# Performance work log

Measured on AMD Instinct MI355X. Metric: run time of the kernel, lower is better.

Reference implementation:

```python
import jax, jax.numpy as jnp
import numpy as np

NPOINT = 1024
RADIUS = 0.2
NSAMPLE = 64
BN_EPS = 1e-5


def setup_inputs() -> dict:
    key = jax.random.key(0)
    ks = jax.random.split(key, 16)
    B, N = 8, 8192
    inp = {
        "xyz": jax.random.normal(ks[0], (B, 3, N), jnp.float32),
        "points": jax.random.normal(ks[1], (B, 3, N), jnp.float32),
        "seed_inds": jax.random.randint(ks[2], (B, N), 0, N),
    }
    chans = [6, 64, 64, 128]
    for i in range(3):
        cin, cout = chans[i], chans[i + 1]
        kk = jax.random.split(ks[3 + i], 3)
        inp[f"w{i}"] = jax.random.normal(kk[0], (cout, cin), jnp.float32) / np.sqrt(cin)
        inp[f"b{i}"] = jnp.zeros((cout,), jnp.float32)
        inp[f"g{i}"] = jnp.ones((cout,), jnp.float32)
        inp[f"be{i}"] = jnp.zeros((cout,), jnp.float32)
        inp[f"m{i}"] = jax.random.normal(kk[1], (cout,), jnp.float32) * 0.1
        inp[f"v{i}"] = jax.random.uniform(kk[2], (cout,), jnp.float32, 0.5, 1.5)
    return inp


def _fps(xyz, npoint):
    # xyz: [B, N, 3]. Deterministic start at index 0 (torch uses a random start).
    B, N, _ = xyz.shape

    def step(carry, _):
        dist, far = carry
        cent = jnp.take_along_axis(xyz, far[:, None, None], axis=1)  # [B,1,3]
        d = jnp.sum((xyz - cent) ** 2, -1)                           # [B,N]
        dist = jnp.minimum(dist, d)
        nxt = jnp.argmax(dist, -1)
        return (dist, nxt), far

    init = (jnp.full((B, N), 1e10, xyz.dtype), jnp.zeros((B,), jnp.int32))
    _, idxs = jax.lax.scan(step, init, None, length=npoint)
    return idxs.T  # [B, npoint]


def _sqdist(src, dst):
    # src [B,S,3], dst [B,N,3] -> [B,S,N]
    d = -2.0 * jnp.einsum("bsc,bnc->bsn", src, dst)
    d += jnp.sum(src ** 2, -1)[:, :, None]
    d += jnp.sum(dst ** 2, -1)[:, None, :]
    return d


def _gather(pts, idx):
    # pts [B,N,C], idx [B,S,K] -> [B,S,K,C]
    B, S, K = idx.shape
    flat = jnp.take_along_axis(pts, idx.reshape(B, S * K, 1), axis=1)
    return flat.reshape(B, S, K, pts.shape[-1])


def _forward(xyz, points, seed_inds, layers):
    xyz_t = xyz.transpose(0, 2, 1)      # [B,N,3]
    pts_t = points.transpose(0, 2, 1)   # [B,N,D]
    B, N, _ = xyz_t.shape

    fps_idx = _fps(xyz_t, NPOINT)                                   # [B,S]
    new_seed = jnp.take_along_axis(seed_inds, fps_idx.astype(seed_inds.dtype), axis=1)
    new_xyz = jnp.take_along_axis(xyz_t, fps_idx[:, :, None], axis=1)  # [B,S,3]

    # ball query via sort trick (same math as torch module)
    sq = _sqdist(new_xyz, xyz_t)                                    # [B,S,N]
    gi = jnp.where(sq > RADIUS ** 2, N, jnp.arange(N, dtype=jnp.int32)[None, None, :])
    gi = jnp.sort(gi, axis=-1)[:, :, :NSAMPLE]                      # [B,S,K]
    first = gi[:, :, :1]
    gi = jnp.where(gi == N, first, gi)

    gxyz = _gather(xyz_t, gi) - new_xyz[:, :, None, :]              # [B,S,K,3]
    gpts = _gather(pts_t, gi)                                       # [B,S,K,D]
    feat = jnp.concatenate([gxyz, gpts], -1)                        # [B,S,K,3+D]

    for (w, b, g, be, m, v) in layers:
        feat = jnp.einsum("bskc,oc->bsko", feat, w) + b             # 1x1 conv
        feat = (feat - m) * (g / jnp.sqrt(v + BN_EPS)) + be         # BN (inference)
        feat = jax.nn.relu(feat)

    new_points = jnp.max(feat, axis=2).transpose(0, 2, 1)           # [B,Cout,S]
    return new_xyz.transpose(0, 2, 1), new_points, new_seed


def reference(xyz, points, seed_inds,
              w0, b0, g0, be0, m0, v0,
              w1, b1, g1, be1, m1, v1,
              w2, b2, g2, be2, m2, v2):
    layers = [(w0, b0, g0, be0, m0, v0),
              (w1, b1, g1, be1, m1, v1),
              (w2, b2, g2, be2, m2, v2)]
    return _forward(xyz, points, seed_inds, layers)
```

## Files before the change

kernel.cpp:

```cpp
#include <hip/hip_runtime.h>

#define B_ 8
#define N_ 8192
#define S_ 1024
#define NS_ 64

typedef float v2f __attribute__((ext_vector_type(2)));
typedef unsigned long long u64;
typedef short bf16x8 __attribute__((ext_vector_type(8)));
typedef float f32x4 __attribute__((ext_vector_type(4)));

#define OUT0 0
#define OUT1 24576
#define OUT2 1073152

template <int CTRL>
static __device__ __forceinline__ float dpp_max_step(float v) {
    int o = __builtin_amdgcn_update_dpp(__float_as_int(v), __float_as_int(v),
                                        CTRL, 0xf, 0xf, false);
    return fmaxf(v, __int_as_float(o));
}
static __device__ __forceinline__ float wave_max_f32(float v) {
    v = dpp_max_step<0x111>(v);
    v = dpp_max_step<0x112>(v);
    v = dpp_max_step<0x114>(v);
    v = dpp_max_step<0x118>(v);
    v = dpp_max_step<0x142>(v);
    v = dpp_max_step<0x143>(v);
    return __int_as_float(__builtin_amdgcn_readlane(__float_as_int(v), 63));
}
template <int CTRL>
static __device__ __forceinline__ unsigned dpp_umin_step(unsigned v) {
    unsigned o = (unsigned)__builtin_amdgcn_update_dpp((int)v, (int)v,
                                                       CTRL, 0xf, 0xf, false);
    return v < o ? v : o;
}
static __device__ __forceinline__ unsigned wave_min_u32(unsigned v) {
    v = dpp_umin_step<0x111>(v);
    v = dpp_umin_step<0x112>(v);
    v = dpp_umin_step<0x114>(v);
    v = dpp_umin_step<0x118>(v);
    v = dpp_umin_step<0x142>(v);
    v = dpp_umin_step<0x143>(v);
    return (unsigned)__builtin_amdgcn_readlane((int)v, 63);
}

static __device__ __forceinline__ short f2bf(float f) {
    unsigned u = __float_as_uint(f);
    return (short)((u + 0x7FFFu + ((u >> 16) & 1u)) >> 16);
}

#define FPS_T 512
#define FPS_J 8

__global__ __launch_bounds__(FPS_T, 1) void fps_kernel(const float* __restrict__ xyz,
                                                       float* out) {
    const int b = blockIdx.x;
    const int t = threadIdx.x;
    const int lane = t & 63;
    const float* X = xyz + b * 3 * N_;

    v2f px2[FPS_J], py2[FPS_J], pz2[FPS_J], dist2[FPS_J];
#pragma unroll
    for (int j = 0; j < FPS_J; ++j) {
        int n = t + 1024 * j;
        px2[j] = (v2f){X[n], X[n + 512]};
        py2[j] = (v2f){X[N_ + n], X[N_ + n + 512]};
        pz2[j] = (v2f){X[2 * N_ + n], X[2 * N_ + n + 512]};
        dist2[j] = (v2f){1e10f, 1e10f};
    }

    __shared__ u64 pairs[2];
    if (t == 0) { pairs[0] = 0ull; pairs[1] = 0ull; }
    __syncthreads();

    float* oseed = out + OUT2 + b * S_;

    int ci = 0;
    float c0 = X[0], c1 = X[N_], c2 = X[2 * N_];

    for (int step = 0; step < S_; ++step) {
        if (t == 0) oseed[step] = __int_as_float(ci);

        v2f mv = (v2f){-1.0f, -1.0f};
        {
#pragma clang fp contract(off)
            v2f c0v = (v2f){c0, c0};
            v2f c1v = (v2f){c1, c1};
            v2f c2v = (v2f){c2, c2};
#pragma unroll
            for (int j = 0; j < FPS_J; ++j) {
                v2f e0 = px2[j] - c0v;
                v2f e1 = py2[j] - c1v;
                v2f e2 = pz2[j] - c2v;
                v2f q0 = e0 * e0;
                v2f q1 = e1 * e1;
                v2f q2 = e2 * e2;
                v2f d  = (q0 + q1) + q2;
                v2f dm = __builtin_elementwise_min(dist2[j], d);
                dist2[j] = dm;
                mv = __builtin_elementwise_max(mv, dm);
            }
        }
        float m = fmaxf(mv.x, mv.y);
        float wmax = wave_max_f32(m);

        unsigned mask = 0u;
#pragma unroll
        for (int j = 0; j < FPS_J; ++j) {
            if (dist2[j].x == wmax) mask |= (1u << (2 * j));
            if (dist2[j].y == wmax) mask |= (1u << (2 * j + 1));
        }
        unsigned cand = 0xffffffffu;
        if (mask) {
            int bit = __ffs(mask) - 1;
            cand = (unsigned)(t + (bit << 9));
        }
        unsigned widx = wave_min_u32(cand);

        if (lane == 0) {
            u64 pv = ((u64)(step + 1) << 45) |
                     ((u64)__float_as_uint(wmax) << 13) |
                     (u64)(8191u - widx);
            atomicMax(&pairs[(step + 1) & 1], pv);
        }
        __syncthreads();

        u64 p = pairs[(step + 1) & 1];
        ci = 8191 - (int)(p & 0x1fffull);
        int cu = __builtin_amdgcn_readfirstlane(ci);
        c0 = X[cu];
        c1 = X[N_ + cu];
        c2 = X[2 * N_ + cu];
    }
}

__global__ __launch_bounds__(256) void gather_kernel(const float* __restrict__ xyz,
                                                     const int* __restrict__ seed,
                                                     float* out) {
    int t = blockIdx.x * 256 + threadIdx.x;
    int b = t >> 10, s = t & 1023;
    int idx = __float_as_int(out[OUT2 + t]) & 8191;
    const float* X = xyz + b * 3 * N_;
    float x = X[idx], y = X[N_ + idx], z = X[2 * N_ + idx];
    out[OUT0 + (b * 3 + 0) * S_ + s] = x;
    out[OUT0 + (b * 3 + 1) * S_ + s] = y;
    out[OUT0 + (b * 3 + 2) * S_ + s] = z;
    out[OUT2 + t] = (float)seed[b * N_ + idx];
}

__global__ __launch_bounds__(256) void ballquery_kernel(const float* __restrict__ xyz,
                                                        float* out) {
    int wid = threadIdx.x >> 6, lane = threadIdx.x & 63;
    int sg = blockIdx.x * 4 + wid;
    int b = sg >> 10, s = sg & 1023;
    const float* X = xyz + b * 3 * N_;
    float c0 = out[OUT0 + (b * 3 + 0) * S_ + s];
    float c1 = out[OUT0 + (b * 3 + 1) * S_ + s];
    float c2 = out[OUT0 + (b * 3 + 2) * S_ + s];
    float* G = out + OUT1 + (b * 128) * S_ + s;

    int cnt = 0, first = 0;
    for (int base = 0; base < N_ && cnt < NS_; base += 128) {
        int n0 = base + lane;
        int n1 = base + 64 + lane;
        float x0 = X[n0], y0 = X[N_ + n0], z0 = X[2 * N_ + n0];
        float x1 = X[n1], y1 = X[N_ + n1], z1 = X[2 * N_ + n1];
        float e0 = x0 - c0, e1 = y0 - c1, e2 = z0 - c2;
        float d0 = fmaf(e2, e2, fmaf(e1, e1, e0 * e0));
        float f0 = x1 - c0, f1 = y1 - c1, f2 = z1 - c2;
        float d1 = fmaf(f2, f2, fmaf(f1, f1, f0 * f0));

        u64 mask0 = __ballot(d0 <= 0.04f);
        if (mask0) {
            if (cnt == 0) first = base + __ffsll(mask0) - 1;
            int pos = cnt + (int)__popcll(mask0 & ((1ull << lane) - 1ull));
            if ((d0 <= 0.04f) && pos < NS_) G[pos * S_] = __int_as_float(n0);
            cnt += (int)__popcll(mask0);
        }
        u64 mask1 = __ballot(d1 <= 0.04f);
        if (mask1) {
            if (cnt == 0) first = base + 64 + __ffsll(mask1) - 1;
            int pos = cnt + (int)__popcll(mask1 & ((1ull << lane) - 1ull));
            if ((d1 <= 0.04f) && pos < NS_) G[pos * S_] = __int_as_float(n1);
            cnt += (int)__popcll(mask1);
        }
    }
    if (lane >= cnt && lane < NS_) G[lane * S_] = __int_as_float(first);
}

__global__ __launch_bounds__(256) void mlp_kernel(
    const float* __restrict__ xyz, const float* __restrict__ pts,
    const float* __restrict__ w0, const float* __restrict__ b0,
    const float* __restrict__ g0, const float* __restrict__ be0,
    const float* __restrict__ m0, const float* __restrict__ v0,
    const float* __restrict__ w1, const float* __restrict__ b1,
    const float* __restrict__ g1, const float* __restrict__ be1,
    const float* __restrict__ m1, const float* __restrict__ v1,
    const float* __restrict__ w2, const float* __restrict__ b2,
    const float* __restrict__ g2, const float* __restrict__ be2,
    const float* __restrict__ m2, const float* __restrict__ v2,
    float* out) {
    const int sg = blockIdx.x;
    const int b = sg >> 10, s = sg & 1023;
    const int t = threadIdx.x;
    const int lane = t & 63;
    const int wq = __builtin_amdgcn_readfirstlane(t >> 6);
    const int ln = lane & 15;
    const int quad = (lane >> 4) & 3;

    __shared__ float f0[64 * 9];
    __shared__ short featA[64 * 72];
    __shared__ short featB[64 * 72];
    __shared__ float wmaxs[4 * 132];
    __shared__ float scs[256], ofs[256];

    {
        float sc, of;
        if (t < 64) {
            int c = t;
            sc = g0[c] / sqrtf(v0[c] + 1e-5f);
            of = (b0[c] - m0[c]) * sc + be0[c];
        } else if (t < 128) {
            int c = t - 64;
            sc = g1[c] / sqrtf(v1[c] + 1e-5f);
            of = (b1[c] - m1[c]) * sc + be1[c];
        } else {
            int c = t - 128;
            sc = g2[c] / sqrtf(v2[c] + 1e-5f);
            of = (b2[c] - m2[c]) * sc + be2[c];
        }
        scs[t] = sc;
        ofs[t] = of;
    }

    if (t < 64) {
        int gidx = __float_as_int(out[OUT1 + (b * 128 + t) * S_ + s]) & 8191;
        const float* X = xyz + b * 3 * N_;
        const float* P = pts + b * 3 * N_;
        float cx = out[OUT0 + (b * 3 + 0) * S_ + s];
        float cy = out[OUT0 + (b * 3 + 1) * S_ + s];
        float cz = out[OUT0 + (b * 3 + 2) * S_ + s];
        f0[t * 9 + 0] = X[gidx] - cx;
        f0[t * 9 + 1] = X[N_ + gidx] - cy;
        f0[t * 9 + 2] = X[2 * N_ + gidx] - cz;
        f0[t * 9 + 3] = P[gidx];
        f0[t * 9 + 4] = P[N_ + gidx];
        f0[t * 9 + 5] = P[2 * N_ + gidx];
    }
    __syncthreads();

    {
        float in[6];
#pragma unroll
        for (int c = 0; c < 6; ++c) in[c] = f0[lane * 9 + c];
#pragma unroll 1
        for (int i = 0; i < 16; i += 4) {
            int o = wq * 16 + i;
            float a0 = 0.f, a1 = 0.f, a2 = 0.f, a3 = 0.f;
#pragma unroll
            for (int c = 0; c < 6; ++c) {
                float rc = in[c];
                a0 = fmaf(rc, w0[(o + 0) * 6 + c], a0);
                a1 = fmaf(rc, w0[(o + 1) * 6 + c], a1);
                a2 = fmaf(rc, w0[(o + 2) * 6 + c], a2);
                a3 = fmaf(rc, w0[(o + 3) * 6 + c], a3);
            }
            featA[lane * 72 + o + 0] = f2bf(fmaxf(fmaf(a0, scs[o + 0], ofs[o + 0]), 0.f));
            featA[lane * 72 + o + 1] = f2bf(fmaxf(fmaf(a1, scs[o + 1], ofs[o + 1]), 0.f));
            featA[lane * 72 + o + 2] = f2bf(fmaxf(fmaf(a2, scs[o + 2], ofs[o + 2]), 0.f));
            featA[lane * 72 + o + 3] = f2bf(fmaxf(fmaf(a3, scs[o + 3], ofs[o + 3]), 0.f));
        }
    }
    __syncthreads();

    const int arow = 16 * wq + ln;

    {
        bf16x8 a1f[2];
#pragma unroll
        for (int ks = 0; ks < 2; ++ks)
            a1f[ks] = *(const bf16x8*)&featA[arow * 72 + ks * 32 + quad * 8];

#pragma unroll
        for (int nt = 0; nt < 4; ++nt) {
            f32x4 acc = {0.f, 0.f, 0.f, 0.f};
#pragma unroll
            for (int ks = 0; ks < 2; ++ks) {
                const float* wr = w1 + (nt * 16 + ln) * 64 + ks * 32 + quad * 8;
                float4 p = *(const float4*)wr;
                float4 q = *(const float4*)(wr + 4);
                bf16x8 bf = {f2bf(p.x), f2bf(p.y), f2bf(p.z), f2bf(p.w),
                             f2bf(q.x), f2bf(q.y), f2bf(q.z), f2bf(q.w)};
                acc = __builtin_amdgcn_mfma_f32_16x16x32_bf16(a1f[ks], bf, acc, 0, 0, 0);
            }
            int o = nt * 16 + ln;
            float sc = scs[64 + o], of = ofs[64 + o];
#pragma unroll
            for (int reg = 0; reg < 4; ++reg) {
                float y = fmaxf(fmaf(acc[reg], sc, of), 0.f);
                featB[(16 * wq + quad * 4 + reg) * 72 + o] = f2bf(y);
            }
        }
    }

    {
        bf16x8 a2f[2];
#pragma unroll
        for (int ks = 0; ks < 2; ++ks)
            a2f[ks] = *(const bf16x8*)&featB[arow * 72 + ks * 32 + quad * 8];

#pragma unroll
        for (int nt = 0; nt < 8; ++nt) {
            f32x4 acc = {0.f, 0.f, 0.f, 0.f};
#pragma unroll
            for (int ks = 0; ks < 2; ++ks) {
                const float* wr = w2 + (nt * 16 + ln) * 64 + ks * 32 + quad * 8;
                float4 p = *(const float4*)wr;
                float4 q = *(const float4*)(wr + 4);
                bf16x8 bf = {f2bf(p.x), f2bf(p.y), f2bf(p.z), f2bf(p.w),
                             f2bf(q.x), f2bf(q.y), f2bf(q.z), f2bf(q.w)};
                acc = __builtin_amdgcn_mfma_f32_16x16x32_bf16(a2f[ks], bf, acc, 0, 0, 0);
            }
            int o = nt * 16 + ln;
            float sc = scs[128 + o], of = ofs[128 + o];
            float m = -1.f;
#pragma unroll
            for (int reg = 0; reg < 4; ++reg) {
                float y = fmaxf(fmaf(acc[reg], sc, of), 0.f);
                m = fmaxf(m, y);
            }
            m = fmaxf(m, __shfl_xor(m, 16, 64));
            m = fmaxf(m, __shfl_xor(m, 32, 64));
            if (lane < 16) wmaxs[wq * 132 + o] = m;
        }
    }
    __syncthreads();

    if (t < 128) {
        float m = fmaxf(fmaxf(wmaxs[0 * 132 + t], wmaxs[1 * 132 + t]),
                        fmaxf(wmaxs[2 * 132 + t], wmaxs[3 * 132 + t]));
        out[OUT1 + (b * 128 + t) * S_ + s] = m;
    }
}

extern "C" void kernel_launch(void* const* d_in, const int* in_sizes, int n_in,
                              void* d_out, int out_size, void* d_ws, size_t ws_size,
                              hipStream_t stream) {
    const float* xyz  = (const float*)d_in[0];
    const float* pts  = (const float*)d_in[1];
    const int*   seed = (const int*)d_in[2];
    const float* w0 = (const float*)d_in[3];
    const float* b0 = (const float*)d_in[4];
    const float* g0 = (const float*)d_in[5];
    const float* be0 = (const float*)d_in[6];
    const float* m0 = (const float*)d_in[7];
    const float* v0 = (const float*)d_in[8];
    const float* w1 = (const float*)d_in[9];
    const float* b1 = (const float*)d_in[10];
    const float* g1 = (const float*)d_in[11];
    const float* be1 = (const float*)d_in[12];
    const float* m1 = (const float*)d_in[13];
    const float* v1 = (const float*)d_in[14];
    const float* w2 = (const float*)d_in[15];
    const float* b2 = (const float*)d_in[16];
    const float* g2 = (const float*)d_in[17];
    const float* be2 = (const float*)d_in[18];
    const float* m2 = (const float*)d_in[19];
    const float* v2 = (const float*)d_in[20];
    float* out = (float*)d_out;
    (void)d_ws; (void)ws_size;

    fps_kernel<<<dim3(B_), dim3(FPS_T), 0, stream>>>(xyz, out);
    gather_kernel<<<dim3(8192 / 256), dim3(256), 0, stream>>>(xyz, seed, out);
    ballquery_kernel<<<dim3(2048), dim3(256), 0, stream>>>(xyz, out);
    mlp_kernel<<<dim3(8192), dim3(256), 0, stream>>>(xyz, pts,
        w0, b0, g0, be0, m0, v0,
        w1, b1, g1, be1, m1, v1,
        w2, b2, g2, be2, m2, v2,
        out);
}
```

Baseline: 1.381 ms.

## Fuse centroid gather and ball query into MLP kernel with 4-wave parallel search

```diff
diff --git a/kernel.cpp b/kernel.cpp
--- a/kernel.cpp
+++ b/kernel.cpp
@@ -135,62 +135,9 @@
     }
 }
 
-__global__ __launch_bounds__(256) void gather_kernel(const float* __restrict__ xyz,
-                                                     const int* __restrict__ seed,
-                                                     float* out) {
-    int t = blockIdx.x * 256 + threadIdx.x;
-    int b = t >> 10, s = t & 1023;
-    int idx = __float_as_int(out[OUT2 + t]) & 8191;
-    const float* X = xyz + b * 3 * N_;
-    float x = X[idx], y = X[N_ + idx], z = X[2 * N_ + idx];
-    out[OUT0 + (b * 3 + 0) * S_ + s] = x;
-    out[OUT0 + (b * 3 + 1) * S_ + s] = y;
-    out[OUT0 + (b * 3 + 2) * S_ + s] = z;
-    out[OUT2 + t] = (float)seed[b * N_ + idx];
-}
-
-__global__ __launch_bounds__(256) void ballquery_kernel(const float* __restrict__ xyz,
-                                                        float* out) {
-    int wid = threadIdx.x >> 6, lane = threadIdx.x & 63;
-    int sg = blockIdx.x * 4 + wid;
-    int b = sg >> 10, s = sg & 1023;
-    const float* X = xyz + b * 3 * N_;
-    float c0 = out[OUT0 + (b * 3 + 0) * S_ + s];
-    float c1 = out[OUT0 + (b * 3 + 1) * S_ + s];
-    float c2 = out[OUT0 + (b * 3 + 2) * S_ + s];
-    float* G = out + OUT1 + (b * 128) * S_ + s;
-
-    int cnt = 0, first = 0;
-    for (int base = 0; base < N_ && cnt < NS_; base += 128) {
-        int n0 = base + lane;
-        int n1 = base + 64 + lane;
-        float x0 = X[n0], y0 = X[N_ + n0], z0 = X[2 * N_ + n0];
-        float x1 = X[n1], y1 = X[N_ + n1], z1 = X[2 * N_ + n1];
-        float e0 = x0 - c0, e1 = y0 - c1, e2 = z0 - c2;
-        float d0 = fmaf(e2, e2, fmaf(e1, e1, e0 * e0));
-        float f0 = x1 - c0, f1 = y1 - c1, f2 = z1 - c2;
-        float d1 = fmaf(f2, f2, fmaf(f1, f1, f0 * f0));
-
-        u64 mask0 = __ballot(d0 <= 0.04f);
-        if (mask0) {
-            if (cnt == 0) first = base + __ffsll(mask0) - 1;
-            int pos = cnt + (int)__popcll(mask0 & ((1ull << lane) - 1ull));
-            if ((d0 <= 0.04f) && pos < NS_) G[pos * S_] = __int_as_float(n0);
-            cnt += (int)__popcll(mask0);
-        }
-        u64 mask1 = __ballot(d1 <= 0.04f);
-        if (mask1) {
-            if (cnt == 0) first = base + 64 + __ffsll(mask1) - 1;
-            int pos = cnt + (int)__popcll(mask1 & ((1ull << lane) - 1ull));
-            if ((d1 <= 0.04f) && pos < NS_) G[pos * S_] = __int_as_float(n1);
-            cnt += (int)__popcll(mask1);
-        }
-    }
-    if (lane >= cnt && lane < NS_) G[lane * S_] = __int_as_float(first);
-}
-
-__global__ __launch_bounds__(256) void mlp_kernel(
+__global__ __launch_bounds__(256) void down_kernel(
     const float* __restrict__ xyz, const float* __restrict__ pts,
+    const int* __restrict__ seed,
     const float* __restrict__ w0, const float* __restrict__ b0,
     const float* __restrict__ g0, const float* __restrict__ be0,
     const float* __restrict__ m0, const float* __restrict__ v0,
@@ -214,6 +161,14 @@
     __shared__ short featB[64 * 72];
     __shared__ float wmaxs[4 * 132];
     __shared__ float scs[256], ofs[256];
+    __shared__ int cand[4 * 64];
+    __shared__ int cnts[4];
+    __shared__ int gis[64];
+
+    const float* X = xyz + b * 3 * N_;
+
+    int ci = __float_as_int(out[OUT2 + sg]) & 8191;
+    float cx = X[ci], cy = X[N_ + ci], cz = X[2 * N_ + ci];
 
     {
         float sc, of;
@@ -233,14 +188,63 @@
         scs[t] = sc;
         ofs[t] = of;
     }
+    __syncthreads();
+
+    if (t == 0) {
+        out[OUT0 + (b * 3 + 0) * S_ + s] = cx;
+        out[OUT0 + (b * 3 + 1) * S_ + s] = cy;
+        out[OUT0 + (b * 3 + 2) * S_ + s] = cz;
+        out[OUT2 + sg] = (float)seed[b * N_ + ci];
+    }
+
+    {
+        int cnt = 0;
+        const int wbase = wq << 11;
+        for (int base = 0; base < 2048 && cnt < NS_; base += 128) {
+            int n0 = wbase + base + lane;
+            int n1 = n0 + 64;
+            float x0 = X[n0], y0 = X[N_ + n0], z0 = X[2 * N_ + n0];
+            float x1 = X[n1], y1 = X[N_ + n1], z1 = X[2 * N_ + n1];
+            float e0 = x0 - cx, e1 = y0 - cy, e2 = z0 - cz;
+            float d0 = fmaf(e2, e2, fmaf(e1, e1, e0 * e0));
+            float q0 = x1 - cx, q1 = y1 - cy, q2 = z1 - cz;
+            float d1 = fmaf(q2, q2, fmaf(q1, q1, q0 * q0));
+
+            u64 mask0 = __ballot(d0 <= 0.04f);
+            if (mask0) {
+                int pos = cnt + (int)__popcll(mask0 & ((1ull << lane) - 1ull));
+                if ((d0 <= 0.04f) && pos < NS_) cand[(wq << 6) + pos] = n0;
+                cnt += (int)__popcll(mask0);
+            }
+            u64 mask1 = __ballot(d1 <= 0.04f);
+            if (mask1) {
+                int pos = cnt + (int)__popcll(mask1 & ((1ull << lane) - 1ull));
+                if ((d1 <= 0.04f) && pos < NS_) cand[(wq << 6) + pos] = n1;
+                cnt += (int)__popcll(mask1);
+            }
+        }
+        if (lane == 0) cnts[wq] = cnt;
+    }
+    __syncthreads();
 
     if (t < 64) {
-        int gidx = __float_as_int(out[OUT1 + (b * 128 + t) * S_ + s]) & 8191;
-        const float* X = xyz + b * 3 * N_;
+        int k = t;
+        int start = 0, sel = -1, firstv = -1;
+#pragma unroll
+        for (int w = 0; w < 4; ++w) {
+            int cw = min(cnts[w], NS_);
+            if (firstv < 0 && cw > 0) firstv = cand[(w << 6)];
+            if (sel < 0 && k < start + cw) sel = cand[(w << 6) + (k - start)];
+            start += cw;
+        }
+        if (sel < 0) sel = firstv;
+        gis[t] = sel;
+    }
+    __syncthreads();
+
+    if (t < 64) {
+        int gidx = gis[t] & 8191;
         const float* P = pts + b * 3 * N_;
-        float cx = out[OUT0 + (b * 3 + 0) * S_ + s];
-        float cy = out[OUT0 + (b * 3 + 1) * S_ + s];
-        float cz = out[OUT0 + (b * 3 + 2) * S_ + s];
         f0[t * 9 + 0] = X[gidx] - cx;
         f0[t * 9 + 1] = X[N_ + gidx] - cy;
         f0[t * 9 + 2] = X[2 * N_ + gidx] - cz;
@@ -372,9 +376,7 @@
     (void)d_ws; (void)ws_size;
 
     fps_kernel<<<dim3(B_), dim3(FPS_T), 0, stream>>>(xyz, out);
-    gather_kernel<<<dim3(8192 / 256), dim3(256), 0, stream>>>(xyz, seed, out);
-    ballquery_kernel<<<dim3(2048), dim3(256), 0, stream>>>(xyz, out);
-    mlp_kernel<<<dim3(8192), dim3(256), 0, stream>>>(xyz, pts,
+    down_kernel<<<dim3(B_ * S_), dim3(256), 0, stream>>>(xyz, pts, seed,
         w0, b0, g0, be0, m0, v0,
         w1, b1, g1, be1, m1, v1,
         w2, b2, g2, be2, m2, v2,
```

Result: no change. 1.376 ms (-0.3%).
